# Performance work log

Measured on AMD Instinct MI355X. Metric: run time of the kernel, lower is better.

Reference implementation:

```python
import jax, jax.numpy as jnp
import numpy as np

B, T, S, D, H, DK = 2, 2048, 2048, 1024, 16, 64


def setup_inputs() -> dict:
    key = jax.random.key(0)
    ks = jax.random.split(key, 11)
    s = 1.0 / np.sqrt(D)
    return {
        "query": jax.random.normal(ks[0], (B, T, D), jnp.float32),
        "value": jax.random.normal(ks[1], (B, S, D), jnp.float32),
        "key": jax.random.normal(ks[2], (B, S, D), jnp.float32),
        "Wq": jax.random.normal(ks[3], (D, H, DK), jnp.float32) * s,
        "bq": jnp.zeros((H, DK), jnp.float32),
        "Wk": jax.random.normal(ks[4], (D, H, DK), jnp.float32) * s,
        "bk": jnp.zeros((H, DK), jnp.float32),
        "Wv": jax.random.normal(ks[5], (D, H, DK), jnp.float32) * s,
        "bv": jnp.zeros((H, DK), jnp.float32),
        "Wo": jax.random.normal(ks[6], (H, DK, D), jnp.float32) * (1.0 / np.sqrt(H * DK)),
        "bo": jnp.zeros((D,), jnp.float32),
    }


def reference(query, value, key, Wq, bq, Wk, bk, Wv, bv, Wo, bo):
    # Projections: (B, seq, D) x (D, H, DK) -> (B, seq, H, DK)
    q = jnp.einsum("btd,dhk->bthk", query, Wq) + bq
    k = jnp.einsum("bsd,dhk->bshk", key, Wk) + bk
    v = jnp.einsum("bsd,dhk->bshk", value, Wv) + bv
    # Scaled dot-product attention (keras scales query by 1/sqrt(key_dim))
    q = q * (1.0 / np.sqrt(DK)).astype(np.float32)
    scores = jnp.einsum("bshk,bthk->bhts", k, q)  # (B, H, T, S)
    probs = jax.nn.softmax(scores, axis=-1)
    attn = jnp.einsum("bhts,bshk->bthk", probs, v)  # (B, T, H, DK)
    # Output projection back to model dim
    out = jnp.einsum("bthk,hkd->btd", attn, Wo) + bo
    return out
```

## Files before the change

### kernel.cpp

```cpp
#include <hip/hip_runtime.h>
#include <math.h>

#define BB  2
#define TT  2048
#define SSQ 2048
#define DD  1024
#define HH  16
#define DKK 64
#define MM  (BB*TT)
#define NN  (HH*DKK)

typedef __attribute__((ext_vector_type(8))) short short8;
typedef __attribute__((ext_vector_type(4))) float f32x4;
typedef __attribute__((ext_vector_type(2))) unsigned int uint2v;
typedef __attribute__((ext_vector_type(4))) unsigned int u32x4;

__device__ __forceinline__ short f2bf(float x) {
    unsigned u = __builtin_bit_cast(unsigned, x);
    unsigned r = (u + 0x7FFFu + ((u >> 16) & 1u)) >> 16;
    return (short)r;
}

__device__ __forceinline__ unsigned pk2(float lo, float hi) {
    return (__builtin_bit_cast(unsigned, hi) & 0xFFFF0000u) |
           (__builtin_bit_cast(unsigned, lo) >> 16);
}

__device__ __forceinline__ void glds16(const void* g, void* l) {
    __builtin_amdgcn_global_load_lds(
        (const __attribute__((address_space(1))) void*)g,
        (__attribute__((address_space(3))) void*)l, 16, 0, 0);
}

__global__ __launch_bounds__(256)
void to_bf16_acts(const float* __restrict__ a0, const float* __restrict__ a1,
                  const float* __restrict__ a2,
                  short* __restrict__ o0, short* __restrict__ o1,
                  short* __restrict__ o2)
{
    int z = blockIdx.y;
    const float* in = (z == 0) ? a0 : (z == 1) ? a1 : a2;
    short* out = (z == 0) ? o0 : (z == 1) ? o1 : o2;
    size_t i0 = ((size_t)blockIdx.x * 256 + threadIdx.x) * 8;
    f32x4 f0 = *(const f32x4*)(in + i0);
    f32x4 f1 = *(const f32x4*)(in + i0 + 4);
    short8 v;
#pragma unroll
    for (int j = 0; j < 4; j++) v[j] = f2bf(f0[j]);
#pragma unroll
    for (int j = 0; j < 4; j++) v[4 + j] = f2bf(f1[j]);
    *(short8*)(out + i0) = v;
}

__global__ __launch_bounds__(256)
void wtrans(const float* __restrict__ w0, const float* __restrict__ w1,
            const float* __restrict__ w2, const float* __restrict__ w3,
            short* __restrict__ t0, short* __restrict__ t1,
            short* __restrict__ t2, short* __restrict__ t3)
{
    __shared__ float Ls[64][65];
    int z = blockIdx.z;
    const float* in = (z == 0) ? w0 : (z == 1) ? w1 : (z == 2) ? w2 : w3;
    short* out = (z == 0) ? t0 : (z == 1) ? t1 : (z == 2) ? t2 : t3;
    const int r0 = blockIdx.y * 64, c0 = blockIdx.x * 64;
    const int t = threadIdx.x;
    const int r = t >> 2, c4 = t & 3;

    const float* src = in + (size_t)(r0 + r) * DD + c0 + c4 * 16;
#pragma unroll
    for (int i = 0; i < 4; i++) {
        f32x4 f = *(const f32x4*)(src + i * 4);
#pragma unroll
        for (int j = 0; j < 4; j++) Ls[r][c4 * 16 + i * 4 + j] = f[j];
    }
    __syncthreads();

    short8 va, vb;
#pragma unroll
    for (int j = 0; j < 8; j++) va[j] = f2bf(Ls[c4 * 16 + j][r]);
#pragma unroll
    for (int j = 0; j < 8; j++) vb[j] = f2bf(Ls[c4 * 16 + 8 + j][r]);
    short* dst = out + (size_t)(c0 + r) * DD + r0 + c4 * 16;
    *(short8*)dst = va;
    *(short8*)(dst + 8) = vb;
}

__global__ __launch_bounds__(256)
void vtrans(const short* __restrict__ in, short* __restrict__ out)
{
    __shared__ short Ls[64][72];
    const int bh = blockIdx.y;
    const int t0 = blockIdx.x * 64;
    const int tid = threadIdx.x;
    const int r = tid >> 2, c4 = tid & 3;

    const short* src = in + ((size_t)bh * TT + t0 + r) * DKK + c4 * 16;
    *(short8*)&Ls[r][c4 * 16]     = *(const short8*)(src);
    *(short8*)&Ls[r][c4 * 16 + 8] = *(const short8*)(src + 8);
    __syncthreads();

    short8 a, b;
#pragma unroll
    for (int j = 0; j < 8; j++) a[j] = Ls[c4 * 16 + j][r];
#pragma unroll
    for (int j = 0; j < 8; j++) b[j] = Ls[c4 * 16 + 8 + j][r];
    short* dst = out + ((size_t)bh * DKK + r) * SSQ + t0 + c4 * 16;
    *(short8*)dst = a;
    *(short8*)(dst + 8) = b;
}

__device__ __forceinline__ void gemm_core(const short* __restrict__ A,
                                          const short* __restrict__ Bt,
                                          int m0, int n0,
                                          short* As, short* Bs,
                                          f32x4 (&acc)[4][4])
{
    const int tid = threadIdx.x;
    const int w = tid >> 6, l = tid & 63;
    const int l15 = l & 15, quad = l >> 4;
    const int wm = w >> 1, wn = w & 1;

#pragma unroll
    for (int i = 0; i < 4; i++)
#pragma unroll
        for (int j = 0; j < 4; j++) acc[i][j] = (f32x4){0.f, 0.f, 0.f, 0.f};

    const int r = tid >> 2, cseg = tid & 3;
    const short* gA = A + (size_t)(m0 + r) * DD + cseg * 8;
    const short* gB = Bt + (size_t)(n0 + r) * DD + cseg * 8;
    short* ldsA = As + w * 512;
    short* ldsB = Bs + w * 512;

    for (int k0 = 0; k0 < DD; k0 += 32) {
        glds16(gA + k0,                 ldsA);
        glds16(gA + (size_t)64 * DD + k0, ldsA + 2048);
        glds16(gB + k0,                 ldsB);
        glds16(gB + (size_t)64 * DD + k0, ldsB + 2048);
        __syncthreads();

        short8 bF[4];
#pragma unroll
        for (int ni = 0; ni < 4; ni++)
            bF[ni] = *(const short8*)&Bs[(wn * 64 + ni * 16 + l15) * 32 + quad * 8];
#pragma unroll
        for (int mi = 0; mi < 4; mi++) {
            short8 aF = *(const short8*)&As[(wm * 64 + mi * 16 + l15) * 32 + quad * 8];
#pragma unroll
            for (int ni = 0; ni < 4; ni++)
                acc[mi][ni] = __builtin_amdgcn_mfma_f32_16x16x32_bf16(aF, bF[ni], acc[mi][ni], 0, 0, 0);
        }
        __syncthreads();
    }
}

__global__ __launch_bounds__(256, 3)
void gemm_qkv(const short* __restrict__ Aq, const short* __restrict__ Ak,
              const short* __restrict__ Av,
              const short* __restrict__ Wqt, const short* __restrict__ Wkt,
              const short* __restrict__ Wvt,
              const float* __restrict__ bq, const float* __restrict__ bk,
              const float* __restrict__ bv,
              short* __restrict__ Qb, short* __restrict__ Kb,
              short* __restrict__ Vtmp)
{
    __shared__ short As[128 * 32];
    __shared__ short Bs[128 * 32];
    const int z = blockIdx.z;
    const short* A  = (z == 0) ? Aq : (z == 1) ? Ak : Av;
    const short* Bt = (z == 0) ? Wqt : (z == 1) ? Wkt : Wvt;
    const float* bias = (z == 0) ? bq : (z == 1) ? bk : bv;
    short* dst = (z == 0) ? Qb : (z == 1) ? Kb : Vtmp;
    const int m0 = blockIdx.y * 128, n0 = blockIdx.x * 128;

    f32x4 acc[4][4];
    gemm_core(A, Bt, m0, n0, As, Bs, acc);

    const int tid = threadIdx.x;
    const int w = tid >> 6, l = tid & 63;
    const int l15 = l & 15, quad = l >> 4;
    const int wm = w >> 1, wn = w & 1;
    const float scale = (z == 0) ? 0.1803368801f : 1.0f;

#pragma unroll
    for (int mi = 0; mi < 4; mi++) {
#pragma unroll
        for (int reg = 0; reg < 4; reg++) {
            int m = m0 + wm * 64 + mi * 16 + quad * 4 + reg;
            int b = m >> 11, t = m & 2047;
#pragma unroll
            for (int ni = 0; ni < 4; ni++) {
                int n = n0 + wn * 64 + ni * 16 + l15;
                float vv = (acc[mi][ni][reg] + bias[n]) * scale;
                int h = n >> 6, dk = n & 63;
                dst[((size_t)(b * HH + h) * TT + t) * DKK + dk] = f2bf(vv);
            }
        }
    }
}

__global__ __launch_bounds__(256, 3)
void gemm_out(const short* __restrict__ Ab, const short* __restrict__ Wot,
              const float* __restrict__ bo, float* __restrict__ out)
{
    __shared__ short As[128 * 32];
    __shared__ short Bs[128 * 32];
    const int m0 = blockIdx.y * 128, n0 = blockIdx.x * 128;

    f32x4 acc[4][4];
    gemm_core(Ab, Wot, m0, n0, As, Bs, acc);

    const int tid = threadIdx.x;
    const int w = tid >> 6, l = tid & 63;
    const int l15 = l & 15, quad = l >> 4;
    const int wm = w >> 1, wn = w & 1;

#pragma unroll
    for (int mi = 0; mi < 4; mi++) {
#pragma unroll
        for (int reg = 0; reg < 4; reg++) {
            int m = m0 + wm * 64 + mi * 16 + quad * 4 + reg;
#pragma unroll
            for (int ni = 0; ni < 4; ni++) {
                int n = n0 + wn * 64 + ni * 16 + l15;
                out[(size_t)m * DD + n] = acc[mi][ni][reg] + bo[n];
            }
        }
    }
}

__global__ __launch_bounds__(256, 3)
void attn_mfma(const short* __restrict__ Qb, const short* __restrict__ Kb,
               const short* __restrict__ Vbt, short* __restrict__ Ab)
{
    __shared__ short KV[2 * 2 * 64 * 72];

    const int tid = threadIdx.x;
    const int w = tid >> 6, l = tid & 63;
    const int l15 = l & 15, quad = l >> 4;

    const int fid = blockIdx.y * 16 + blockIdx.x;
    const int swz = (fid & 7) * 64 + (fid >> 3);
    const int t0 = (swz & 15) * 128;
    const int bh = swz >> 4;
    const size_t hb = (size_t)bh * SSQ * DKK;
    const int r = tid >> 2, c4 = tid & 3;

    short8 qf[2][2];
#pragma unroll
    for (int mf = 0; mf < 2; mf++)
#pragma unroll
        for (int kk = 0; kk < 2; kk++)
            qf[mf][kk] = *(const short8*)(Qb + hb +
                (size_t)(t0 + 32 * w + 16 * mf + l15) * DKK + kk * 32 + quad * 8);

    const short* gkb = Kb + hb + (size_t)r * DKK + c4 * 16;
    const short* gvb = Vbt + hb + (size_t)r * SSQ + c4 * 16;
    short8 kr0 = *(const short8*)(gkb + 0);
    short8 kr1 = *(const short8*)(gkb + 8);
    short8 vr0 = *(const short8*)(gvb + 0);
    short8 vr1 = *(const short8*)(gvb + 8);

    f32x4 o[2][4];
#pragma unroll
    for (int mf = 0; mf < 2; mf++)
#pragma unroll
        for (int j = 0; j < 4; j++) o[mf][j] = (f32x4){0.f, 0.f, 0.f, 0.f};
    float lsum[2] = {0.f, 0.f};

    short* skb = KV + r * 72 + c4 * 16;

    for (int s0 = 0; s0 < SSQ; s0 += 64) {
        const int dbo = (s0 & 64) ? 9216 : 0;
        *(short8*)(skb + dbo)          = kr0;
        *(short8*)(skb + dbo + 8)      = kr1;
        *(short8*)(skb + dbo + 4608)   = vr0;
        *(short8*)(skb + dbo + 4616)   = vr1;
        if (s0 + 64 < SSQ) {
            const short* gk = gkb + (size_t)(s0 + 64) * DKK;
            const short* gv = gvb + (s0 + 64);
            kr0 = *(const short8*)(gk + 0);
            kr1 = *(const short8*)(gk + 8);
            vr0 = *(const short8*)(gv + 0);
            vr1 = *(const short8*)(gv + 8);
        }
        __syncthreads();
        const short* kb_ = KV + dbo;
        const short* vb_ = kb_ + 4608;

        f32x4 sc[4][2];
#pragma unroll
        for (int np = 0; np < 4; np++)
#pragma unroll
            for (int mf = 0; mf < 2; mf++) sc[np][mf] = (f32x4){0.f, 0.f, 0.f, 0.f};
        __builtin_amdgcn_s_setprio(1);
#pragma unroll
        for (int kk = 0; kk < 2; kk++) {
#pragma unroll
            for (int np = 0; np < 4; np++) {
                short8 aK = *(const short8*)&kb_[(16 * np + l15) * 72 + kk * 32 + quad * 8];
                sc[np][0] = __builtin_amdgcn_mfma_f32_16x16x32_bf16(aK, qf[0][kk], sc[np][0], 0, 0, 0);
                sc[np][1] = __builtin_amdgcn_mfma_f32_16x16x32_bf16(aK, qf[1][kk], sc[np][1], 0, 0, 0);
            }
        }
        __builtin_amdgcn_s_setprio(0);

        short8 pa[2][2];
#pragma unroll
        for (int mf = 0; mf < 2; mf++) {
            float ls = lsum[mf];
#pragma unroll
            for (int kk = 0; kk < 2; kk++) {
                u32x4 wd;
#pragma unroll
                for (int b = 0; b < 2; b++) {
                    float p00 = __builtin_amdgcn_exp2f(sc[2 * kk][mf][2 * b]);
                    float p01 = __builtin_amdgcn_exp2f(sc[2 * kk][mf][2 * b + 1]);
                    float p10 = __builtin_amdgcn_exp2f(sc[2 * kk + 1][mf][2 * b]);
                    float p11 = __builtin_amdgcn_exp2f(sc[2 * kk + 1][mf][2 * b + 1]);
                    ls += (p00 + p01) + (p10 + p11);
                    unsigned Xw = pk2(p00, p01);
                    unsigned Yw = pk2(p10, p11);
                    uint2v s1 = __builtin_amdgcn_permlane32_swap(Xw, Yw, false, false);
                    uint2v s2 = __builtin_amdgcn_permlane16_swap(s1[0], s1[1], false, false);
                    wd[b]     = s2[0];
                    wd[2 + b] = s2[1];
                }
                pa[mf][kk] = __builtin_bit_cast(short8, wd);
            }
            lsum[mf] = ls;
        }

        __builtin_amdgcn_s_setprio(1);
#pragma unroll
        for (int kk = 0; kk < 2; kk++) {
#pragma unroll
            for (int np = 0; np < 4; np++) {
                short8 bV = *(const short8*)&vb_[(16 * np + l15) * 72 + kk * 32 + quad * 8];
                o[0][np] = __builtin_amdgcn_mfma_f32_16x16x32_bf16(pa[0][kk], bV, o[0][np], 0, 0, 0);
                o[1][np] = __builtin_amdgcn_mfma_f32_16x16x32_bf16(pa[1][kk], bV, o[1][np], 0, 0, 0);
            }
        }
        __builtin_amdgcn_s_setprio(0);
    }

    const int b = bh >> 4, h = bh & 15;
#pragma unroll
    for (int mf = 0; mf < 2; mf++) {
        float ls = lsum[mf];
        ls += __shfl_xor(ls, 16);
        ls += __shfl_xor(ls, 32);
        float inv = 1.f / ls;
#pragma unroll
        for (int reg = 0; reg < 4; reg++) {
            float invr = __shfl(inv, quad * 4 + reg);
            int t = t0 + 32 * w + 16 * mf + quad * 4 + reg;
#pragma unroll
            for (int np = 0; np < 4; np++) {
                Ab[((size_t)(b * TT + t) * HH + h) * DKK + 16 * np + l15] =
                    f2bf(o[mf][np][reg] * invr);
            }
        }
    }
}

extern "C" void kernel_launch(void* const* d_in, const int* in_sizes, int n_in,
                              void* d_out, int out_size, void* d_ws, size_t ws_size,
                              hipStream_t stream)
{
    const float* query = (const float*)d_in[0];
    const float* value = (const float*)d_in[1];
    const float* key   = (const float*)d_in[2];
    const float* Wq    = (const float*)d_in[3];
    const float* bq    = (const float*)d_in[4];
    const float* Wk    = (const float*)d_in[5];
    const float* bk    = (const float*)d_in[6];
    const float* Wv    = (const float*)d_in[7];
    const float* bv    = (const float*)d_in[8];
    const float* Wo    = (const float*)d_in[9];
    const float* bo    = (const float*)d_in[10];
    float* out = (float*)d_out;

    const size_t actE = (size_t)MM * DD;
    const size_t wE   = (size_t)DD * NN;
    short* p = (short*)d_ws;
    short* Aq   = p; p += actE;
    short* Ak   = p; p += actE;
    short* Av   = p; p += actE;
    short* Wqt  = p; p += wE;
    short* Wkt  = p; p += wE;
    short* Wvt  = p; p += wE;
    short* Wot  = p; p += wE;
    short* Qb   = p; p += actE;
    short* Kb   = p; p += actE;
    short* Vtmp = p; p += actE;
    short* Vbt  = p; p += actE;
    short* Ab   = p; p += actE;

    dim3 blk(256);

    to_bf16_acts<<<dim3((unsigned)(actE / 2048), 3), blk, 0, stream>>>(
        query, key, value, Aq, Ak, Av);

    wtrans<<<dim3(16, 16, 4), blk, 0, stream>>>(Wq, Wk, Wv, Wo, Wqt, Wkt, Wvt, Wot);

    gemm_qkv<<<dim3(NN / 128, MM / 128, 3), blk, 0, stream>>>(
        Aq, Ak, Av, Wqt, Wkt, Wvt, bq, bk, bv, Qb, Kb, Vtmp);

    vtrans<<<dim3(TT / 64, BB * HH), blk, 0, stream>>>(Vtmp, Vbt);

    attn_mfma<<<dim3(TT / 128, BB * HH), blk, 0, stream>>>(Qb, Kb, Vbt, Ab);

    gemm_out<<<dim3(DD / 128, MM / 128), blk, 0, stream>>>(Ab, Wot, bo, out);
}
```

Before: 233.8 us.

## Split attention over key halves, combine in a separate kernel, shrink out-GEMM tile

The attention kernel now splits the key/value sequence into two halves on a third grid dimension, doubling the block count for better occupancy. Each half writes unnormalized fp32 partial outputs and row sums, computed with an MFMA against a ones vector. A new combine_norm kernel adds the halves, normalizes and converts to bf16. The output GEMM uses 64x128 tiles to launch more blocks. The cost is an extra launch, extra fp32 traffic through reused workspace buffers, and the split relies on no max-subtraction being done, so the partial sums add exactly.

Result: faster. 228.0 us (-2.5%).

```diff
diff --git a/kernel.cpp b/kernel.cpp
--- a/kernel.cpp
+++ b/kernel.cpp
@@ -202,23 +202,51 @@
 void gemm_out(const short* __restrict__ Ab, const short* __restrict__ Wot,
               const float* __restrict__ bo, float* __restrict__ out)
 {
-    __shared__ short As[128 * 32];
+    __shared__ short As[64 * 32];
     __shared__ short Bs[128 * 32];
-    const int m0 = blockIdx.y * 128, n0 = blockIdx.x * 128;
-
-    f32x4 acc[4][4];
-    gemm_core(Ab, Wot, m0, n0, As, Bs, acc);
-
+    const int m0 = blockIdx.y * 64, n0 = blockIdx.x * 128;
     const int tid = threadIdx.x;
     const int w = tid >> 6, l = tid & 63;
     const int l15 = l & 15, quad = l >> 4;
     const int wm = w >> 1, wn = w & 1;
 
-#pragma unroll
-    for (int mi = 0; mi < 4; mi++) {
+    f32x4 acc[2][4];
+#pragma unroll
+    for (int i = 0; i < 2; i++)
+#pragma unroll
+        for (int j = 0; j < 4; j++) acc[i][j] = (f32x4){0.f, 0.f, 0.f, 0.f};
+
+    const int r = tid >> 2, cseg = tid & 3;
+    const short* gA = Ab + (size_t)(m0 + r) * DD + cseg * 8;
+    const short* gB = Wot + (size_t)(n0 + r) * DD + cseg * 8;
+    short* ldsA = As + w * 512;
+    short* ldsB = Bs + w * 512;
+
+    for (int k0 = 0; k0 < DD; k0 += 32) {
+        glds16(gA + k0,                   ldsA);
+        glds16(gB + k0,                   ldsB);
+        glds16(gB + (size_t)64 * DD + k0, ldsB + 2048);
+        __syncthreads();
+
+        short8 bF[4];
+#pragma unroll
+        for (int ni = 0; ni < 4; ni++)
+            bF[ni] = *(const short8*)&Bs[(wn * 64 + ni * 16 + l15) * 32 + quad * 8];
+#pragma unroll
+        for (int mi = 0; mi < 2; mi++) {
+            short8 aF = *(const short8*)&As[(wm * 32 + mi * 16 + l15) * 32 + quad * 8];
+#pragma unroll
+            for (int ni = 0; ni < 4; ni++)
+                acc[mi][ni] = __builtin_amdgcn_mfma_f32_16x16x32_bf16(aF, bF[ni], acc[mi][ni], 0, 0, 0);
+        }
+        __syncthreads();
+    }
+
+#pragma unroll
+    for (int mi = 0; mi < 2; mi++) {
 #pragma unroll
         for (int reg = 0; reg < 4; reg++) {
-            int m = m0 + wm * 64 + mi * 16 + quad * 4 + reg;
+            int m = m0 + wm * 32 + mi * 16 + quad * 4 + reg;
 #pragma unroll
             for (int ni = 0; ni < 4; ni++) {
                 int n = n0 + wn * 64 + ni * 16 + l15;
@@ -228,9 +256,11 @@
     }
 }
 
-__global__ __launch_bounds__(256, 3)
+__global__ __launch_bounds__(256, 4)
 void attn_mfma(const short* __restrict__ Qb, const short* __restrict__ Kb,
-               const short* __restrict__ Vbt, short* __restrict__ Ab)
+               const short* __restrict__ Vbt,
+               float* __restrict__ O1, float* __restrict__ O2,
+               float* __restrict__ l1, float* __restrict__ l2)
 {
     __shared__ short KV[2 * 2 * 64 * 72];
 
@@ -242,8 +272,10 @@
     const int swz = (fid & 7) * 64 + (fid >> 3);
     const int t0 = (swz & 15) * 128;
     const int bh = swz >> 4;
+    const int half = blockIdx.z;
     const size_t hb = (size_t)bh * SSQ * DKK;
     const int r = tid >> 2, c4 = tid & 3;
+    const int sbase = half * 1024;
 
     short8 qf[2][2];
 #pragma unroll
@@ -253,8 +285,8 @@
             qf[mf][kk] = *(const short8*)(Qb + hb +
                 (size_t)(t0 + 32 * w + 16 * mf + l15) * DKK + kk * 32 + quad * 8);
 
-    const short* gkb = Kb + hb + (size_t)r * DKK + c4 * 16;
-    const short* gvb = Vbt + hb + (size_t)r * SSQ + c4 * 16;
+    const short* gkb = Kb + hb + (size_t)(sbase + r) * DKK + c4 * 16;
+    const short* gvb = Vbt + hb + (size_t)r * SSQ + sbase + c4 * 16;
     short8 kr0 = *(const short8*)(gkb + 0);
     short8 kr1 = *(const short8*)(gkb + 8);
     short8 vr0 = *(const short8*)(gvb + 0);
@@ -265,17 +297,19 @@
     for (int mf = 0; mf < 2; mf++)
 #pragma unroll
         for (int j = 0; j < 4; j++) o[mf][j] = (f32x4){0.f, 0.f, 0.f, 0.f};
-    float lsum[2] = {0.f, 0.f};
+    f32x4 lacc[2] = {(f32x4){0.f, 0.f, 0.f, 0.f}, (f32x4){0.f, 0.f, 0.f, 0.f}};
+    const short8 ones = {(short)0x3F80, (short)0x3F80, (short)0x3F80, (short)0x3F80,
+                         (short)0x3F80, (short)0x3F80, (short)0x3F80, (short)0x3F80};
 
     short* skb = KV + r * 72 + c4 * 16;
 
-    for (int s0 = 0; s0 < SSQ; s0 += 64) {
+    for (int s0 = 0; s0 < 1024; s0 += 64) {
         const int dbo = (s0 & 64) ? 9216 : 0;
         *(short8*)(skb + dbo)          = kr0;
         *(short8*)(skb + dbo + 8)      = kr1;
         *(short8*)(skb + dbo + 4608)   = vr0;
         *(short8*)(skb + dbo + 4616)   = vr1;
-        if (s0 + 64 < SSQ) {
+        if (s0 + 64 < 1024) {
             const short* gk = gkb + (size_t)(s0 + 64) * DKK;
             const short* gv = gvb + (s0 + 64);
             kr0 = *(const short8*)(gk + 0);
@@ -307,7 +341,6 @@
         short8 pa[2][2];
 #pragma unroll
         for (int mf = 0; mf < 2; mf++) {
-            float ls = lsum[mf];
 #pragma unroll
             for (int kk = 0; kk < 2; kk++) {
                 u32x4 wd;
@@ -317,7 +350,6 @@
                     float p01 = __builtin_amdgcn_exp2f(sc[2 * kk][mf][2 * b + 1]);
                     float p10 = __builtin_amdgcn_exp2f(sc[2 * kk + 1][mf][2 * b]);
                     float p11 = __builtin_amdgcn_exp2f(sc[2 * kk + 1][mf][2 * b + 1]);
-                    ls += (p00 + p01) + (p10 + p11);
                     unsigned Xw = pk2(p00, p01);
                     unsigned Yw = pk2(p10, p11);
                     uint2v s1 = __builtin_amdgcn_permlane32_swap(Xw, Yw, false, false);
@@ -327,12 +359,13 @@
                 }
                 pa[mf][kk] = __builtin_bit_cast(short8, wd);
             }
-            lsum[mf] = ls;
         }
 
         __builtin_amdgcn_s_setprio(1);
 #pragma unroll
         for (int kk = 0; kk < 2; kk++) {
+            lacc[0] = __builtin_amdgcn_mfma_f32_16x16x32_bf16(pa[0][kk], ones, lacc[0], 0, 0, 0);
+            lacc[1] = __builtin_amdgcn_mfma_f32_16x16x32_bf16(pa[1][kk], ones, lacc[1], 0, 0, 0);
 #pragma unroll
             for (int np = 0; np < 4; np++) {
                 short8 bV = *(const short8*)&vb_[(16 * np + l15) * 72 + kk * 32 + quad * 8];
@@ -343,24 +376,45 @@
         __builtin_amdgcn_s_setprio(0);
     }
 
-    const int b = bh >> 4, h = bh & 15;
+    float* O = half ? O2 : O1;
+    float* L = half ? l2 : l1;
+    const size_t rowb = (size_t)bh * TT;
 #pragma unroll
     for (int mf = 0; mf < 2; mf++) {
-        float ls = lsum[mf];
-        ls += __shfl_xor(ls, 16);
-        ls += __shfl_xor(ls, 32);
-        float inv = 1.f / ls;
 #pragma unroll
         for (int reg = 0; reg < 4; reg++) {
-            float invr = __shfl(inv, quad * 4 + reg);
             int t = t0 + 32 * w + 16 * mf + quad * 4 + reg;
-#pragma unroll
-            for (int np = 0; np < 4; np++) {
-                Ab[((size_t)(b * TT + t) * HH + h) * DKK + 16 * np + l15] =
-                    f2bf(o[mf][np][reg] * invr);
-            }
-        }
-    }
+            if (l15 == 0) L[rowb + t] = lacc[mf][reg];
+            float* orow = O + (rowb + t) * DKK;
+#pragma unroll
+            for (int np = 0; np < 4; np++)
+                orow[16 * np + l15] = o[mf][np][reg];
+        }
+    }
+}
+
+__global__ __launch_bounds__(256)
+void combine_norm(const float* __restrict__ O1, const float* __restrict__ O2,
+                  const float* __restrict__ l1, const float* __restrict__ l2,
+                  short* __restrict__ Ab)
+{
+    size_t g = (size_t)blockIdx.x * 256 + threadIdx.x;
+    size_t i0 = g * 8;
+    int bh = (int)(i0 >> 17);
+    int t  = (int)((i0 >> 6) & 2047);
+    int dk = (int)(i0 & 63);
+    float inv = 1.f / (l1[(size_t)bh * TT + t] + l2[(size_t)bh * TT + t]);
+    f32x4 a0 = *(const f32x4*)(O1 + i0);
+    f32x4 a1 = *(const f32x4*)(O1 + i0 + 4);
+    f32x4 b0 = *(const f32x4*)(O2 + i0);
+    f32x4 b1 = *(const f32x4*)(O2 + i0 + 4);
+    short8 v;
+#pragma unroll
+    for (int j = 0; j < 4; j++) v[j] = f2bf((a0[j] + b0[j]) * inv);
+#pragma unroll
+    for (int j = 0; j < 4; j++) v[4 + j] = f2bf((a1[j] + b1[j]) * inv);
+    int b = bh >> 4, h = bh & 15;
+    *(short8*)(Ab + (((size_t)(b * TT + t) * HH + h) * DKK + dk)) = v;
 }
 
 extern "C" void kernel_launch(void* const* d_in, const int* in_sizes, int n_in,
@@ -395,6 +449,10 @@
     short* Vtmp = p; p += actE;
     short* Vbt  = p; p += actE;
     short* Ab   = p; p += actE;
+    float* O2f  = (float*)p; p += 2 * actE;
+    float* O1f  = (float*)Aq;
+    float* l1f  = (float*)Av;
+    float* l2f  = l1f + (size_t)BB * HH * TT;
 
     dim3 blk(256);
 
@@ -408,7 +466,11 @@
 
     vtrans<<<dim3(TT / 64, BB * HH), blk, 0, stream>>>(Vtmp, Vbt);
 
-    attn_mfma<<<dim3(TT / 128, BB * HH), blk, 0, stream>>>(Qb, Kb, Vbt, Ab);
-
-    gemm_out<<<dim3(DD / 128, MM / 128), blk, 0, stream>>>(Ab, Wot, bo, out);
-}
+    attn_mfma<<<dim3(TT / 128, BB * HH, 2), blk, 0, stream>>>(
+        Qb, Kb, Vbt, O1f, O2f, l1f, l2f);
+
+    combine_norm<<<dim3((unsigned)(actE / 2048)), blk, 0, stream>>>(
+        O1f, O2f, l1f, l2f, Ab);
+
+    gemm_out<<<dim3(NN / 128, MM / 64), blk, 0, stream>>>(Ab, Wot, bo, out);
+}
```
